# Kernel tuning notes

Hardware: AMD Instinct MI355X
Metric: run time of the kernel (lower is better)

## Reference

```python
import jax, jax.numpy as jnp
import numpy as np

N_QUBITS = 4
N_LAYERS = 3
B = 65536
EPS = 1e-5  # BatchNorm1d default eps

CNOT = jnp.array([[1, 0, 0, 0],
                  [0, 1, 0, 0],
                  [0, 0, 0, 1],
                  [0, 0, 1, 0]], dtype=jnp.complex64)


def _apply_1q(state, U, q):
    # state: [B, 2,2,2,2]; U: [2,2] (shared) or [B,2,2] (per-sample)
    s = jnp.moveaxis(state, 1 + q, -1)
    if U.ndim == 3:
        s = jnp.einsum('b...j,bij->b...i', s, U)
    else:
        s = jnp.einsum('...j,ij->...i', s, U)
    return jnp.moveaxis(s, -1, 1 + q)


def _apply_cnot(state, c, t):
    s = jnp.moveaxis(state, (1 + c, 1 + t), (-2, -1))
    shp = s.shape
    s = jnp.einsum('...j,ij->...i', s.reshape(shp[:-2] + (4,)), CNOT)
    return jnp.moveaxis(s.reshape(shp), (-2, -1), (1 + c, 1 + t))


def _rx_batched(theta):  # theta: [B] -> [B,2,2]
    c = jnp.cos(theta / 2).astype(jnp.complex64)
    s = (-1j * jnp.sin(theta / 2).astype(jnp.complex64))
    return jnp.stack([jnp.stack([c, s], -1), jnp.stack([s, c], -1)], -2)


def _ry(theta):  # scalar -> [2,2]
    c = jnp.cos(theta / 2).astype(jnp.complex64)
    s = jnp.sin(theta / 2).astype(jnp.complex64)
    return jnp.stack([jnp.stack([c, -s]), jnp.stack([s, c])])


def _rz(theta):  # scalar -> [2,2] diagonal
    e = jnp.exp(-1j * theta.astype(jnp.complex64) / 2)
    z = jnp.zeros_like(e)
    return jnp.stack([jnp.stack([e, z]), jnp.stack([z, jnp.conj(e)])])


def _circuit(angles, qparams):
    bsz = angles.shape[0]
    state = jnp.zeros((bsz, 2 ** N_QUBITS), jnp.complex64).at[:, 0].set(1.0)
    state = state.reshape((bsz,) + (2,) * N_QUBITS)
    for q in range(N_QUBITS):
        state = _apply_1q(state, _rx_batched(angles[:, q]), q)
    for l in range(N_LAYERS):
        for q in range(N_QUBITS):
            state = _apply_1q(state, _ry(qparams[l, q, 0]), q)
            state = _apply_1q(state, _rz(qparams[l, q, 1]), q)
        for q in range(N_QUBITS - 1):
            state = _apply_cnot(state, q, q + 1)
        state = _apply_cnot(state, N_QUBITS - 1, 0)
    probs = jnp.abs(state) ** 2  # [B,2,2,2,2]
    zs = []
    for q in range(N_QUBITS):
        axes = tuple(a for a in range(1, N_QUBITS + 1) if a != 1 + q)
        p = probs.sum(axes)  # [B,2]
        zs.append(p[:, 0] - p[:, 1])
    return jnp.stack(zs, -1)  # [B, n_qubits]


def setup_inputs() -> dict:
    key = jax.random.key(0)
    k1, k2, k3 = jax.random.split(key, 3)
    x = jax.random.normal(k1, (B, 1, 24, 24), dtype=jnp.float32)
    enc_w = 0.1 * jax.random.normal(k2, (N_QUBITS, 16), dtype=jnp.float32)
    enc_b = jnp.zeros((N_QUBITS,), jnp.float32)
    qparams = 0.01 * jax.random.normal(k3, (N_LAYERS, N_QUBITS, 3), dtype=jnp.float32)
    gamma = jnp.ones((N_QUBITS,), jnp.float32)
    beta = jnp.zeros((N_QUBITS,), jnp.float32)
    return {"x": x, "enc_w": enc_w, "enc_b": enc_b, "qparams": qparams,
            "gamma": gamma, "beta": beta}


def reference(x, enc_w, enc_b, qparams, gamma, beta):
    bsz = x.shape[0]
    # avg_pool2d(kernel=6, stride=6): [B,1,24,24] -> [B,1,4,4] -> [B,16]
    pooled = x.reshape(bsz, 1, 4, 6, 4, 6).mean((3, 5)).reshape(bsz, 16)
    angles = pooled @ enc_w.T + enc_b  # [B, n_qubits]
    out = _circuit(angles, qparams)    # [B, n_qubits]
    # BatchNorm1d (training mode: batch stats, biased var)
    mean = out.mean(0)
    var = out.var(0)
    return (out - mean) / jnp.sqrt(var + EPS) * gamma + beta
```

## Files before the change

kernel.cpp:

```cpp
#include <hip/hip_runtime.h>
#include <math.h>


#define BATCH 65536
#define SPW 8
#define MAIN_BLOCKS (BATCH / (4 * SPW))

__global__ __launch_bounds__(256) void qnat_precompute(const float* __restrict__ qp,
                                                       float* __restrict__ A) {
  __shared__ float Ur[16][17], Ui[16][17];
  const int tid = threadIdx.x;
  if (tid < 16) {
    const int col = tid;
    float ur[16], ui[16];
#pragma unroll
    for (int i = 0; i < 16; i++) { ur[i] = (i == col) ? 1.f : 0.f; ui[i] = 0.f; }
#pragma unroll
    for (int l = 0; l < 3; l++) {
#pragma unroll
      for (int q = 0; q < 4; q++) {
        const int b = 3 - q;
        const float ty = qp[(l * 4 + q) * 3 + 0];
        const float tz = qp[(l * 4 + q) * 3 + 1];
        const float cy = cosf(0.5f * ty), sy = sinf(0.5f * ty);
#pragma unroll
        for (int i0 = 0; i0 < 16; i0++) {
          if (((i0 >> b) & 1) == 0) {
            const int i1 = i0 | (1 << b);
            const float r0 = ur[i0], m0 = ui[i0], r1 = ur[i1], m1 = ui[i1];
            ur[i0] = cy * r0 - sy * r1;  ui[i0] = cy * m0 - sy * m1;
            ur[i1] = sy * r0 + cy * r1;  ui[i1] = sy * m0 + cy * m1;
          }
        }
        const float cz = cosf(0.5f * tz), sz = sinf(0.5f * tz);
#pragma unroll
        for (int i0 = 0; i0 < 16; i0++) {
          if (((i0 >> b) & 1) == 0) {
            const int i1 = i0 | (1 << b);
            const float r0 = ur[i0], m0 = ui[i0], r1 = ur[i1], m1 = ui[i1];
            ur[i0] = cz * r0 + sz * m0;  ui[i0] = cz * m0 - sz * r0;
            ur[i1] = cz * r1 - sz * m1;  ui[i1] = cz * m1 + sz * r1;
          }
        }
      }
      const int cb[4] = {3, 2, 1, 0};
      const int tb[4] = {2, 1, 0, 3};
#pragma unroll
      for (int e = 0; e < 4; e++) {
#pragma unroll
        for (int i = 0; i < 16; i++) {
          if (((i >> cb[e]) & 1) && (((i >> tb[e]) & 1) == 0)) {
            const int j2 = i | (1 << tb[e]);
            float t0 = ur[i]; ur[i] = ur[j2]; ur[j2] = t0;
            float t1 = ui[i]; ui[i] = ui[j2]; ui[j2] = t1;
          }
        }
      }
    }
#pragma unroll
    for (int i = 0; i < 16; i++) { Ur[i][col] = ur[i]; Ui[i][col] = ui[i]; }
  }
  __syncthreads();
  const int j = tid >> 4, k = tid & 15;
#pragma unroll
  for (int q = 0; q < 4; q++) {
    const int b = 3 - q;
    float mr = 0.f, mi = 0.f;
#pragma unroll
    for (int i = 0; i < 16; i++) {
      const float z = ((i >> b) & 1) ? -1.f : 1.f;
      const float ar = Ur[i][j], ai = Ui[i][j], br = Ur[i][k], bi = Ui[i][k];
      mr += z * (ar * br + ai * bi);
      mi += z * (ar * bi - ai * br);
    }
    const int e = (__popc((unsigned)j) - __popc((unsigned)k)) & 3;
    const float re = (e == 0) ? mr : (e == 1) ? -mi : (e == 2) ? -mr : mi;
    A[(q << 8) + tid] = re;
  }
}

__global__ __launch_bounds__(256) void qnat_main(const float* __restrict__ x,
                                                 const float* __restrict__ enc_w,
                                                 const float* __restrict__ enc_b,
                                                 const float* __restrict__ A,
                                                 float* __restrict__ out) {
  __shared__ float4 sW4[16];
  const int tid = threadIdx.x;
  if (tid < 16) {
    const float inv36 = 1.0f / 36.0f;
    sW4[tid] = make_float4(enc_w[tid] * inv36, enc_w[16 + tid] * inv36,
                           enc_w[32 + tid] * inv36, enc_w[48 + tid] * inv36);
  }
  __syncthreads();

  const int wave = tid >> 6, lane = tid & 63;
  const int j = lane & 15;
  const int g = lane >> 4;

  float4 w4[9];
#pragma unroll
  for (int t = 0; t < 9; t++) {
    const int p = lane + 64 * t;
    const int row = p / 24, colp = p - row * 24;
    const int fidx = (row / 6) * 4 + (colp / 6);
    w4[t] = sW4[fidx];
  }
  float Areg[16];
#pragma unroll
  for (int k = 0; k < 16; k++) Areg[k] = A[(g << 8) + (j << 4) + k];
  const float b0 = enc_b[0], b1 = enc_b[1], b2 = enc_b[2], b3 = enc_b[3];

  const int s0 = (blockIdx.x * 4 + wave) * SPW;

  float xv[9];
  {
    const float* xs = x + (size_t)s0 * 576 + lane;
#pragma unroll
    for (int t = 0; t < 9; t++) xv[t] = xs[64 * t];
  }

  for (int i = 0; i < SPW; i++) {
    const int s = s0 + i;
    float xn[9];
    if (i + 1 < SPW) {
      const float* xs = x + (size_t)(s + 1) * 576 + lane;
#pragma unroll
      for (int t = 0; t < 9; t++) xn[t] = xs[64 * t];
    }

    float a0 = 0.f, a1 = 0.f, a2 = 0.f, a3 = 0.f;
#pragma unroll
    for (int t = 0; t < 9; t++) {
      a0 = fmaf(xv[t], w4[t].x, a0);
      a1 = fmaf(xv[t], w4[t].y, a1);
      a2 = fmaf(xv[t], w4[t].z, a2);
      a3 = fmaf(xv[t], w4[t].w, a3);
    }
#pragma unroll
    for (int off = 32; off >= 1; off >>= 1) {
      a0 += __shfl_xor(a0, off);
      a1 += __shfl_xor(a1, off);
      a2 += __shfl_xor(a2, off);
      a3 += __shfl_xor(a3, off);
    }
    const float th0 = a0 + b0, th1 = a1 + b1, th2 = a2 + b2, th3 = a3 + b3;
    float c0, s0_, c1, s1_, c2, s2_, c3, s3_;
    __sincosf(0.5f * th0, &s0_, &c0);
    __sincosf(0.5f * th1, &s1_, &c1);
    __sincosf(0.5f * th2, &s2_, &c2);
    __sincosf(0.5f * th3, &s3_, &c3);
    const float p01[4] = {c0 * c1, c0 * s1_, s0_ * c1, s0_ * s1_};
    const float p23[4] = {c2 * c3, c2 * s3_, s2_ * c3, s2_ * s3_};
    float inner = 0.f;
#pragma unroll
    for (int hi = 0; hi < 4; hi++) {
      float sh = 0.f;
#pragma unroll
      for (int lo = 0; lo < 4; lo++) sh = fmaf(Areg[4 * hi + lo], p23[lo], sh);
      inner = fmaf(p01[hi], sh, inner);
    }
    const float rj = ((j & 8) ? s0_ : c0) * ((j & 4) ? s1_ : c1) *
                     ((j & 2) ? s2_ : c2) * ((j & 1) ? s3_ : c3);
    float v = inner * rj;
    v += __shfl_xor(v, 1);
    v += __shfl_xor(v, 2);
    v += __shfl_xor(v, 4);
    v += __shfl_xor(v, 8);
    if (j == 0) out[(size_t)s * 4 + g] = v;

    if (i + 1 < SPW) {
#pragma unroll
      for (int t = 0; t < 9; t++) xv[t] = xn[t];
    }
  }
}

__global__ __launch_bounds__(256) void qnat_reduce(const float* __restrict__ out,
                                                   double* __restrict__ acc) {
  const int tid = threadIdx.x;
  double s = 0.0, ss = 0.0;
  for (size_t i = (size_t)blockIdx.x * 256 + tid; i < (size_t)BATCH * 4; i += 64 * 256) {
    const double v = (double)out[i];
    s += v;
    ss = fma(v, v, ss);
  }
#pragma unroll
  for (int off = 4; off <= 32; off <<= 1) {
    s += __shfl_xor(s, off);
    ss += __shfl_xor(ss, off);
  }
  __shared__ double sm[2][4][4];
  const int lane = tid & 63, wave = tid >> 6;
  if (lane < 4) { sm[0][wave][lane] = s; sm[1][wave][lane] = ss; }
  __syncthreads();
  if (tid < 4) {
    const double ts = sm[0][0][tid] + sm[0][1][tid] + sm[0][2][tid] + sm[0][3][tid];
    const double tss = sm[1][0][tid] + sm[1][1][tid] + sm[1][2][tid] + sm[1][3][tid];
    atomicAdd(&acc[tid], ts);
    atomicAdd(&acc[4 + tid], tss);
  }
}

__global__ __launch_bounds__(256) void qnat_norm(float* __restrict__ out,
                                                 const double* __restrict__ acc,
                                                 const float* __restrict__ gamma,
                                                 const float* __restrict__ beta) {
  __shared__ float sMean[4], sScale[4], sBeta[4];
  const int tid = threadIdx.x;
  if (tid < 4) {
    const double n = (double)BATCH;
    const double mean = acc[tid] / n;
    const double var = acc[4 + tid] / n - mean * mean;
    const double inv = 1.0 / sqrt(var + 1e-5);
    sMean[tid] = (float)mean;
    sScale[tid] = (float)(gamma[tid] * inv);
    sBeta[tid] = beta[tid];
  }
  __syncthreads();
  const size_t i = (size_t)blockIdx.x * 256 + tid;
  float4 v = ((const float4*)out)[i];
  v.x = (v.x - sMean[0]) * sScale[0] + sBeta[0];
  v.y = (v.y - sMean[1]) * sScale[1] + sBeta[1];
  v.z = (v.z - sMean[2]) * sScale[2] + sBeta[2];
  v.w = (v.w - sMean[3]) * sScale[3] + sBeta[3];
  ((float4*)out)[i] = v;
}

extern "C" void kernel_launch(void* const* d_in, const int* in_sizes, int n_in,
                              void* d_out, int out_size, void* d_ws, size_t ws_size,
                              hipStream_t stream) {
  const float* x       = (const float*)d_in[0];
  const float* enc_w   = (const float*)d_in[1];
  const float* enc_b   = (const float*)d_in[2];
  const float* qparams = (const float*)d_in[3];
  const float* gamma   = (const float*)d_in[4];
  const float* beta    = (const float*)d_in[5];
  float* out = (float*)d_out;

  float* A = (float*)d_ws;
  double* acc = (double*)((char*)d_ws + 4096);

  hipMemsetAsync((char*)d_ws + 4096, 0, 8 * sizeof(double), stream);
  qnat_precompute<<<1, 256, 0, stream>>>(qparams, A);
  qnat_main<<<MAIN_BLOCKS, 256, 0, stream>>>(x, enc_w, enc_b, A, out);
  qnat_reduce<<<64, 256, 0, stream>>>(out, acc);
  qnat_norm<<<256, 256, 0, stream>>>(out, acc, gamma, beta);
}
```

Before: 57.17 us.

## Fuse batch-stat reduction into main kernel, vectorize x loads, drop memset

Moves the per-feature sum and sum-of-squares accumulation into qnat_main using per-block shared reduction and double atomics. This removes the separate reduce kernel and the memset launch; the accumulator is now zeroed inside the precompute kernel. It also switches the per-sample x loads to float4 (three vector loads per lane, the third only on 16 lanes) with reorganised weights, and adds an occupancy hint to launch_bounds. The cost is more atomics contending on the same eight addresses and some extra register pressure in the main kernel.

```diff
diff --git a/kernel.cpp b/kernel.cpp
--- a/kernel.cpp
+++ b/kernel.cpp
@@ -7,9 +7,11 @@
 #define MAIN_BLOCKS (BATCH / (4 * SPW))
 
 __global__ __launch_bounds__(256) void qnat_precompute(const float* __restrict__ qp,
-                                                       float* __restrict__ A) {
+                                                       float* __restrict__ A,
+                                                       double* __restrict__ acc) {
   __shared__ float Ur[16][17], Ui[16][17];
   const int tid = threadIdx.x;
+  if (tid >= 64 && tid < 72) acc[tid - 64] = 0.0;
   if (tid < 16) {
     const int col = tid;
     float ur[16], ui[16];
@@ -79,12 +81,14 @@
   }
 }
 
-__global__ __launch_bounds__(256) void qnat_main(const float* __restrict__ x,
-                                                 const float* __restrict__ enc_w,
-                                                 const float* __restrict__ enc_b,
-                                                 const float* __restrict__ A,
-                                                 float* __restrict__ out) {
+__global__ __launch_bounds__(256, 4) void qnat_main(const float* __restrict__ x,
+                                                    const float* __restrict__ enc_w,
+                                                    const float* __restrict__ enc_b,
+                                                    const float* __restrict__ A,
+                                                    float* __restrict__ out,
+                                                    double* __restrict__ acc) {
   __shared__ float4 sW4[16];
+  __shared__ double sAcc[4][4][2];
   const int tid = threadIdx.x;
   if (tid < 16) {
     const float inv36 = 1.0f / 36.0f;
@@ -97,13 +101,17 @@
   const int j = lane & 15;
   const int g = lane >> 4;
 
-  float4 w4[9];
-#pragma unroll
-  for (int t = 0; t < 9; t++) {
-    const int p = lane + 64 * t;
-    const int row = p / 24, colp = p - row * 24;
-    const int fidx = (row / 6) * 4 + (colp / 6);
-    w4[t] = sW4[fidx];
+  float4 w[3][4];
+#pragma unroll
+  for (int t = 0; t < 3; t++) {
+#pragma unroll
+    for (int c = 0; c < 4; c++) {
+      int p = t * 256 + 4 * lane + c;
+      if (p > 575) p = 575;
+      const int row = p / 24, colp = p - row * 24;
+      const int fidx = (row / 6) * 4 + (colp / 6);
+      w[t][c] = sW4[fidx];
+    }
   }
   float Areg[16];
 #pragma unroll
@@ -111,31 +119,35 @@
   const float b0 = enc_b[0], b1 = enc_b[1], b2 = enc_b[2], b3 = enc_b[3];
 
   const int s0 = (blockIdx.x * 4 + wave) * SPW;
-
-  float xv[9];
-  {
-    const float* xs = x + (size_t)s0 * 576 + lane;
-#pragma unroll
-    for (int t = 0; t < 9; t++) xv[t] = xs[64 * t];
-  }
+  double sd = 0.0, ssd = 0.0;
+
+#define LOADS(S, V0, V1, V2)                                              \
+  {                                                                       \
+    const float4* p4 = (const float4*)(x + (size_t)(S) * 576);            \
+    V0 = p4[lane];                                                        \
+    V1 = p4[64 + lane];                                                   \
+    V2 = (lane < 16) ? p4[128 + lane] : make_float4(0.f, 0.f, 0.f, 0.f);  \
+  }
+
+  float4 xv0, xv1, xv2;
+  LOADS(s0, xv0, xv1, xv2);
 
   for (int i = 0; i < SPW; i++) {
     const int s = s0 + i;
-    float xn[9];
-    if (i + 1 < SPW) {
-      const float* xs = x + (size_t)(s + 1) * 576 + lane;
-#pragma unroll
-      for (int t = 0; t < 9; t++) xn[t] = xs[64 * t];
-    }
+    float4 xn0, xn1, xn2;
+    if (i + 1 < SPW) LOADS(s + 1, xn0, xn1, xn2);
 
     float a0 = 0.f, a1 = 0.f, a2 = 0.f, a3 = 0.f;
-#pragma unroll
-    for (int t = 0; t < 9; t++) {
-      a0 = fmaf(xv[t], w4[t].x, a0);
-      a1 = fmaf(xv[t], w4[t].y, a1);
-      a2 = fmaf(xv[t], w4[t].z, a2);
-      a3 = fmaf(xv[t], w4[t].w, a3);
-    }
+#define ACC1(XS, T, C)                      \
+    a0 = fmaf(XS, w[T][C].x, a0);           \
+    a1 = fmaf(XS, w[T][C].y, a1);           \
+    a2 = fmaf(XS, w[T][C].z, a2);           \
+    a3 = fmaf(XS, w[T][C].w, a3);
+#define ACC4(V, T) ACC1(V.x, T, 0) ACC1(V.y, T, 1) ACC1(V.z, T, 2) ACC1(V.w, T, 3)
+    ACC4(xv0, 0) ACC4(xv1, 1) ACC4(xv2, 2)
+#undef ACC4
+#undef ACC1
+
 #pragma unroll
     for (int off = 32; off >= 1; off >>= 1) {
       a0 += __shfl_xor(a0, off);
@@ -166,38 +178,22 @@
     v += __shfl_xor(v, 2);
     v += __shfl_xor(v, 4);
     v += __shfl_xor(v, 8);
-    if (j == 0) out[(size_t)s * 4 + g] = v;
-
-    if (i + 1 < SPW) {
-#pragma unroll
-      for (int t = 0; t < 9; t++) xv[t] = xn[t];
-    }
-  }
-}
-
-__global__ __launch_bounds__(256) void qnat_reduce(const float* __restrict__ out,
-                                                   double* __restrict__ acc) {
-  const int tid = threadIdx.x;
-  double s = 0.0, ss = 0.0;
-  for (size_t i = (size_t)blockIdx.x * 256 + tid; i < (size_t)BATCH * 4; i += 64 * 256) {
-    const double v = (double)out[i];
-    s += v;
-    ss = fma(v, v, ss);
-  }
-#pragma unroll
-  for (int off = 4; off <= 32; off <<= 1) {
-    s += __shfl_xor(s, off);
-    ss += __shfl_xor(ss, off);
-  }
-  __shared__ double sm[2][4][4];
-  const int lane = tid & 63, wave = tid >> 6;
-  if (lane < 4) { sm[0][wave][lane] = s; sm[1][wave][lane] = ss; }
-  __syncthreads();
-  if (tid < 4) {
-    const double ts = sm[0][0][tid] + sm[0][1][tid] + sm[0][2][tid] + sm[0][3][tid];
-    const double tss = sm[1][0][tid] + sm[1][1][tid] + sm[1][2][tid] + sm[1][3][tid];
-    atomicAdd(&acc[tid], ts);
-    atomicAdd(&acc[4 + tid], tss);
+    if (j == 0) {
+      out[(size_t)s * 4 + g] = v;
+      sd += (double)v;
+      ssd = fma((double)v, (double)v, ssd);
+    }
+
+    if (i + 1 < SPW) { xv0 = xn0; xv1 = xn1; xv2 = xn2; }
+  }
+#undef LOADS
+
+  if (j == 0) { sAcc[wave][g][0] = sd; sAcc[wave][g][1] = ssd; }
+  __syncthreads();
+  if (tid < 8) {
+    const int q = tid & 3, m = tid >> 2;
+    const double t = sAcc[0][q][m] + sAcc[1][q][m] + sAcc[2][q][m] + sAcc[3][q][m];
+    atomicAdd(&acc[m * 4 + q], t);
   }
 }
 
@@ -240,9 +236,7 @@
   float* A = (float*)d_ws;
   double* acc = (double*)((char*)d_ws + 4096);
 
-  hipMemsetAsync((char*)d_ws + 4096, 0, 8 * sizeof(double), stream);
-  qnat_precompute<<<1, 256, 0, stream>>>(qparams, A);
-  qnat_main<<<MAIN_BLOCKS, 256, 0, stream>>>(x, enc_w, enc_b, A, out);
-  qnat_reduce<<<64, 256, 0, stream>>>(out, acc);
+  qnat_precompute<<<1, 256, 0, stream>>>(qparams, A, acc);
+  qnat_main<<<MAIN_BLOCKS, 256, 0, stream>>>(x, enc_w, enc_b, A, out, acc);
   qnat_norm<<<256, 256, 0, stream>>>(out, acc, gamma, beta);
 }
```

Result: no change. 58.04 us (+1.5%).
